# Performance work log

Measured on AMD Instinct MI355X. Metric: run time of the kernel, lower is better.

The kernel has to match this reference:

```python
import jax, jax.numpy as jnp
import numpy as np

HIDDEN = 768
NHEADS = 12
HEAD = HIDDEN // NHEADS


def setup_inputs() -> dict:
    key = jax.random.key(0)
    ks = jax.random.split(key, 10)
    B, S = 32, 512
    s = 1.0 / np.sqrt(HIDDEN)
    return {
        "x": jax.random.normal(ks[0], (B, S, HIDDEN), jnp.float32),
        "additive_attention_mask": jnp.zeros((B, 1, 1, S), jnp.float32),
        "Wq": jax.random.normal(ks[1], (HIDDEN, HIDDEN), jnp.float32) * s,
        "bq": jnp.zeros((HIDDEN,), jnp.float32),
        "Wk": jax.random.normal(ks[2], (HIDDEN, HIDDEN), jnp.float32) * s,
        "bk": jnp.zeros((HIDDEN,), jnp.float32),
        "Wv": jax.random.normal(ks[3], (HIDDEN, HIDDEN), jnp.float32) * s,
        "bv": jnp.zeros((HIDDEN,), jnp.float32),
        "Wo": jax.random.normal(ks[4], (HIDDEN, HIDDEN), jnp.float32) * s,
        "bo": jnp.zeros((HIDDEN,), jnp.float32),
    }


def reference(x, additive_attention_mask, Wq, bq, Wk, bk, Wv, bv, Wo, bo):
    B, S, _ = x.shape
    # projections (dropout is identity in eval mode)
    q = (x @ Wq + bq).reshape(B, S, NHEADS, HEAD)
    k = (x @ Wk + bk).reshape(B, S, NHEADS, HEAD)
    v = (x @ Wv + bv).reshape(B, S, NHEADS, HEAD)
    scores = jnp.einsum('bqhd,bkhd->bhqk', q, k) / jnp.sqrt(jnp.float32(HEAD))
    scores = scores + additive_attention_mask  # broadcast [B,1,1,S]
    probs = jax.nn.softmax(scores, axis=-1)
    attn = jnp.einsum('bhqk,bkhd->bqhd', probs, v).reshape(B, S, HIDDEN)
    return attn @ Wo + bo
```

## Files before the change

### kernel.cpp

```cpp
#include <hip/hip_runtime.h>
#include <stdint.h>

typedef unsigned short u16;
typedef __attribute__((ext_vector_type(4))) float floatx4;
typedef __attribute__((ext_vector_type(8))) __bf16 bf16x8;

__device__ __forceinline__ u16 f2bf(float f) {
  uint32_t u = __float_as_uint(f);
  u += 0x7FFFu + ((u >> 16) & 1u);
  return (u16)(u >> 16);
}

__global__ __launch_bounds__(256) void cast_x_kernel(const float* __restrict__ x,
                                                     u16* __restrict__ out) {
  int i = blockIdx.x * 256 + threadIdx.x;
  const float4* p = (const float4*)x;
  float4 a = p[(size_t)i * 2];
  float4 b = p[(size_t)i * 2 + 1];
  uint32_t w0 = (uint32_t)f2bf(a.x) | ((uint32_t)f2bf(a.y) << 16);
  uint32_t w1 = (uint32_t)f2bf(a.z) | ((uint32_t)f2bf(a.w) << 16);
  uint32_t w2 = (uint32_t)f2bf(b.x) | ((uint32_t)f2bf(b.y) << 16);
  uint32_t w3 = (uint32_t)f2bf(b.z) | ((uint32_t)f2bf(b.w) << 16);
  *(uint4*)(out + (size_t)i * 8) = make_uint4(w0, w1, w2, w3);
}

__global__ __launch_bounds__(256) void prep_wqkv_kernel(
    const float* __restrict__ Wq, const float* __restrict__ Wk, const float* __restrict__ Wv,
    const float* __restrict__ bq, const float* __restrict__ bk, const float* __restrict__ bv,
    u16* __restrict__ Wt, float* __restrict__ bias) {
  int id = blockIdx.x * 256 + threadIdx.x;
  int n = id / 768, k = id - n * 768;
  const float* W; const float* bs; int nn;
  if (n < 768)       { W = Wq; bs = bq; nn = n; }
  else if (n < 1536) { W = Wk; bs = bk; nn = n - 768; }
  else               { W = Wv; bs = bv; nn = n - 1536; }
  Wt[id] = f2bf(W[(size_t)k * 768 + nn]);
  if (k == 0) bias[n] = bs[nn];
}

__global__ __launch_bounds__(256) void prep_wo_kernel(const float* __restrict__ Wo,
                                                      u16* __restrict__ Wt) {
  int id = blockIdx.x * 256 + threadIdx.x;
  int n = id / 768, k = id - n * 768;
  Wt[id] = f2bf(Wo[(size_t)k * 768 + n]);
}

__device__ __forceinline__ void gload16(const void* g, void* l) {
  __builtin_amdgcn_global_load_lds((const __attribute__((address_space(1))) void*)g,
                                   (__attribute__((address_space(3))) void*)l,
                                   16, 0, 0);
}

template <int OUTF32>
__global__ __launch_bounds__(256) void gemm_bt_kernel(
    const u16* __restrict__ A, const u16* __restrict__ Bt,
    const float* __restrict__ bias, void* __restrict__ Cv, int ldc) {
  __shared__ __align__(16) u16 Alds[128 * 32];
  __shared__ __align__(16) u16 Blds[128 * 32];
  const int m0 = blockIdx.x * 128, n0 = blockIdx.y * 128;
  const int tid = threadIdx.x;
  const int lane = tid & 63, wid = tid >> 6;
  const int wr = wid >> 1, wc = wid & 1;
  const int l15 = lane & 15, l4 = lane >> 4;

  floatx4 zz = {0.f, 0.f, 0.f, 0.f};
  floatx4 acc[4][4];
#pragma unroll
  for (int i = 0; i < 4; ++i)
#pragma unroll
    for (int j = 0; j < 4; ++j) acc[i][j] = zz;

  for (int kt = 0; kt < 768; kt += 32) {
#pragma unroll
    for (int c = 0; c < 2; ++c) {
      int idx = (wid * 2 + c) * 64 + lane;
      int row = idx >> 2, kc = idx & 3;
      gload16(A + (size_t)(m0 + row) * 768 + kt + kc * 8,
              (char*)Alds + (wid * 2 + c) * 1024);
      gload16(Bt + (size_t)(n0 + row) * 768 + kt + kc * 8,
              (char*)Blds + (wid * 2 + c) * 1024);
    }
    __syncthreads();
    bf16x8 af[4], bfr[4];
#pragma unroll
    for (int i = 0; i < 4; ++i) {
      af[i]  = *(const bf16x8*)&Alds[(wr * 64 + i * 16 + l15) * 32 + l4 * 8];
      bfr[i] = *(const bf16x8*)&Blds[(wc * 64 + i * 16 + l15) * 32 + l4 * 8];
    }
#pragma unroll
    for (int i = 0; i < 4; ++i)
#pragma unroll
      for (int j = 0; j < 4; ++j)
        acc[i][j] = __builtin_amdgcn_mfma_f32_16x16x32_bf16(af[i], bfr[j], acc[i][j], 0, 0, 0);
    __syncthreads();
  }

#pragma unroll
  for (int i = 0; i < 4; ++i) {
    int row = m0 + wr * 64 + i * 16 + l4 * 4;
#pragma unroll
    for (int j = 0; j < 4; ++j) {
      int col = n0 + wc * 64 + j * 16 + l15;
      float bv = bias[col];
#pragma unroll
      for (int r = 0; r < 4; ++r) {
        float v = acc[i][j][r] + bv;
        if (OUTF32) ((float*)Cv)[(size_t)(row + r) * ldc + col] = v;
        else        ((u16*)Cv)[(size_t)(row + r) * ldc + col] = f2bf(v);
      }
    }
  }
}

__global__ __launch_bounds__(512, 4) void attn_kernel(const u16* __restrict__ qkv,
                                                      const float* __restrict__ mask,
                                                      u16* __restrict__ ctx) {
  __shared__ __align__(16) char lds[34816];
  char* sK = lds;
  char* sV = lds + 16384;
  float* sM = (float*)(lds + 32768);

  const int bid = blockIdx.x;
  const int wg = (bid & 7) * 192 + (bid >> 3);
  const int qt = wg & 3;
  const int h = (wg >> 2) % 12;
  const int b = wg / 48;

  const int tid = threadIdx.x;
  const int lane = tid & 63, w = tid >> 6;
  const int l15 = lane & 15, l4 = lane >> 4;
  const int hi = lane >> 3, doct = lane & 7;

  const u16* base = qkv + (size_t)b * 512 * 2304 + h * 64;
  const u16* Qg = base;
  const u16* Kg = base + 768;
  const u16* Vg = base + 1536;

  const int csw = doct ^ hi;
  const int vp_ = w * 8 + hi;

  auto stageK = [&](int t) {
    const u16* src = Kg + (size_t)(t * 128 + w * 16) * 2304;
#pragma unroll
    for (int i = 0; i < 2; ++i)
      gload16(src + (size_t)(i * 8 + hi) * 2304 + csw * 8,
              sK + (w * 2 + i) * 1024);
  };
  uint4 vra, vrb;
  auto loadV = [&](int t) {
    const u16* vp = Vg + (size_t)(t * 128 + vp_ * 2) * 2304 + doct * 8;
    vra = *(const uint4*)vp;
    vrb = *(const uint4*)(vp + 2304);
  };
  auto writeV = [&]() {
    const u16* pa = (const u16*)&vra;
    const u16* pb = (const u16*)&vrb;
#pragma unroll
    for (int j = 0; j < 8; ++j) {
      int d = doct * 8 + j;
      uint32_t val = (uint32_t)pa[j] | ((uint32_t)pb[j] << 16);
      *(uint32_t*)(sV + d * 256 +
                   ((4 * vp_) ^ ((d & 7) << 4) ^ (((d >> 3) & 3) << 5))) = val;
    }
  };

  float mval = mask[(size_t)b * 512 + tid];
  stageK(0);
  loadV(0);
  const u16* qp = Qg + (size_t)(qt * 128 + w * 16 + l15) * 2304 + l4 * 8;
  bf16x8 qf0 = *(const bf16x8*)qp;
  bf16x8 qf1 = *(const bf16x8*)(qp + 32);
  sM[tid] = mval;
  writeV();
  asm volatile("s_waitcnt vmcnt(0) lgkmcnt(0)" ::: "memory");
  __builtin_amdgcn_sched_barrier(0);
  __builtin_amdgcn_s_barrier();

  floatx4 zz = {0.f, 0.f, 0.f, 0.f};
  floatx4 oacc[4];
#pragma unroll
  for (int da = 0; da < 4; ++da) oacc[da] = zz;
  float m_ = -1e30f, l_ = 0.f;

  const int kswz = (l15 & 7) << 4;
  const int src0 = l15 + 32 * (l4 & 1);
  const int src1 = src0 + 16;
  const bool csel = (l4 & 2) != 0;

  for (int t = 0; t < 4; ++t) {
    if (t < 3) loadV(t + 1);

    floatx4 sacc[8];
#pragma unroll
    for (int ct = 0; ct < 8; ++ct) sacc[ct] = zz;
#pragma unroll
    for (int ct = 0; ct < 8; ++ct) {
      const char* kr = sK + (ct * 16 + l15) * 128;
      bf16x8 k0 = *(const bf16x8*)(kr + ((16 * l4) ^ kswz));
      bf16x8 k1 = *(const bf16x8*)(kr + ((64 + 16 * l4) ^ kswz));
      sacc[ct] = __builtin_amdgcn_mfma_f32_16x16x32_bf16(k0, qf0, sacc[ct], 0, 0, 0);
      sacc[ct] = __builtin_amdgcn_mfma_f32_16x16x32_bf16(k1, qf1, sacc[ct], 0, 0, 0);
    }

    float pm = -1e30f;
#pragma unroll
    for (int ct = 0; ct < 8; ++ct) {
      floatx4 mv = *(const floatx4*)(sM + t * 128 + ct * 16 + l4 * 4);
#pragma unroll
      for (int j = 0; j < 4; ++j) {
        float v = sacc[ct][j] * 0.125f + mv[j];
        sacc[ct][j] = v;
        pm = fmaxf(pm, v);
      }
    }
    pm = fmaxf(pm, __shfl_xor(pm, 16, 64));
    pm = fmaxf(pm, __shfl_xor(pm, 32, 64));
    float nm = fmaxf(m_, pm);
    float sc = __expf(m_ - nm);
    m_ = nm;
    float ts = 0.f;
#pragma unroll
    for (int ct = 0; ct < 8; ++ct)
#pragma unroll
      for (int j = 0; j < 4; ++j) {
        float e = __expf(sacc[ct][j] - nm);
        sacc[ct][j] = e;
        ts += e;
      }
    ts += __shfl_xor(ts, 16, 64);
    ts += __shfl_xor(ts, 32, 64);
    l_ = l_ * sc + ts;
#pragma unroll
    for (int da = 0; da < 4; ++da)
#pragma unroll
      for (int j = 0; j < 4; ++j) oacc[da][j] *= sc;

    uint32_t pk[8][2];
#pragma unroll
    for (int ct = 0; ct < 8; ++ct) {
#pragma unroll
      for (int p = 0; p < 2; ++p) {
        uint32_t ua = __float_as_uint(sacc[ct][2 * p]) + 0x8000u;
        uint32_t ub = __float_as_uint(sacc[ct][2 * p + 1]) + 0x8000u;
        pk[ct][p] = (ua >> 16) | (ub & 0xFFFF0000u);
      }
    }

#pragma unroll
    for (int ks = 0; ks < 4; ++ks) {
      uint32_t A0 = __shfl((int)pk[2 * ks][0], src0, 64);
      uint32_t B0 = __shfl((int)pk[2 * ks + 1][0], src0, 64);
      uint32_t A1 = __shfl((int)pk[2 * ks][1], src0, 64);
      uint32_t B1 = __shfl((int)pk[2 * ks + 1][1], src0, 64);
      uint32_t A2 = __shfl((int)pk[2 * ks][0], src1, 64);
      uint32_t B2 = __shfl((int)pk[2 * ks + 1][0], src1, 64);
      uint32_t A3 = __shfl((int)pk[2 * ks][1], src1, 64);
      uint32_t B3 = __shfl((int)pk[2 * ks + 1][1], src1, 64);
      union { uint32_t u[4]; bf16x8 v; } pf;
      pf.u[0] = csel ? B0 : A0;
      pf.u[1] = csel ? B1 : A1;
      pf.u[2] = csel ? B2 : A2;
      pf.u[3] = csel ? B3 : A3;
#pragma unroll
      for (int da = 0; da < 4; ++da) {
        int dd = da * 16 + l15;
        bf16x8 vf = *(const bf16x8*)(sV + dd * 256 +
            ((64 * ks + 16 * l4) ^ ((dd & 7) << 4) ^ (((dd >> 3) & 3) << 5)));
        oacc[da] = __builtin_amdgcn_mfma_f32_16x16x32_bf16(vf, pf.v, oacc[da], 0, 0, 0);
      }
    }

    asm volatile("s_waitcnt lgkmcnt(0)" ::: "memory");
    __builtin_amdgcn_sched_barrier(0);
    __builtin_amdgcn_s_barrier();
    if (t < 3) {
      stageK(t + 1);
      writeV();
      asm volatile("s_waitcnt vmcnt(0) lgkmcnt(0)" ::: "memory");
      __builtin_amdgcn_sched_barrier(0);
      __builtin_amdgcn_s_barrier();
    }
  }

  float rl = 1.0f / l_;
  u16* op = ctx + ((size_t)b * 512 + qt * 128 + w * 16 + l15) * 768 + h * 64;
#pragma unroll
  for (int da = 0; da < 4; ++da) {
    ushort4 o;
    o.x = f2bf(oacc[da][0] * rl);
    o.y = f2bf(oacc[da][1] * rl);
    o.z = f2bf(oacc[da][2] * rl);
    o.w = f2bf(oacc[da][3] * rl);
    *(ushort4*)(op + da * 16 + l4 * 4) = o;
  }
}

extern "C" void kernel_launch(void* const* d_in, const int* in_sizes, int n_in,
                              void* d_out, int out_size, void* d_ws, size_t ws_size,
                              hipStream_t stream) {
  const float* x    = (const float*)d_in[0];
  const float* mask = (const float*)d_in[1];
  const float* Wq   = (const float*)d_in[2];
  const float* bq   = (const float*)d_in[3];
  const float* Wk   = (const float*)d_in[4];
  const float* bk   = (const float*)d_in[5];
  const float* Wv   = (const float*)d_in[6];
  const float* bv   = (const float*)d_in[7];
  const float* Wo   = (const float*)d_in[8];
  const float* bo   = (const float*)d_in[9];
  float* out = (float*)d_out;

  char* ws = (char*)d_ws;
  u16*   xb   = (u16*)ws;
  u16*   ctx  = (u16*)(ws + 25165824);
  u16*   qkv  = (u16*)(ws + 50331648);
  u16*   wtq  = (u16*)(ws + 125829120);
  u16*   wto  = (u16*)(ws + 129368064);
  float* bqkv = (float*)(ws + 130547712);

  cast_x_kernel<<<6144, 256, 0, stream>>>(x, xb);
  prep_wqkv_kernel<<<6912, 256, 0, stream>>>(Wq, Wk, Wv, bq, bk, bv, wtq, bqkv);
  prep_wo_kernel<<<2304, 256, 0, stream>>>(Wo, wto);
  gemm_bt_kernel<0><<<dim3(128, 18), 256, 0, stream>>>(xb, wtq, bqkv, (void*)qkv, 2304);
  attn_kernel<<<dim3(1536), dim3(512), 0, stream>>>(qkv, mask, ctx);
  gemm_bt_kernel<1><<<dim3(128, 6), 256, 0, stream>>>(ctx, wto, bo, (void*)out, 768);
}
```

Measured before the change: 190.6 us.

## Replace GEMM with 256x256-tile, 4-stage pipelined, swizzled-LDS kernel

Replaces the 128x128 single-buffered GEMM with a 256x256 tile kernel of 512 threads. It uses a 4-deep ring of LDS buffers filled by direct global-to-LDS loads, prefetches three k-tiles ahead, and waits with explicit vmcnt so loads overlap MFMA work. It also adds an XOR swizzle on LDS chunks to avoid bank conflicts, XCD-aware block remapping, and raised s_setprio around the MFMA bursts. The larger tiles give more data reuse per load, but they use 128KB of LDS per block and more accumulator registers, and they leave fewer blocks for the 768-wide output projection (192 blocks).

```diff
diff --git a/kernel.cpp b/kernel.cpp
--- a/kernel.cpp
+++ b/kernel.cpp
@@ -52,59 +52,99 @@
 }
 
 template <int OUTF32>
-__global__ __launch_bounds__(256) void gemm_bt_kernel(
+__global__ __launch_bounds__(512, 2) void gemm256_kernel(
     const u16* __restrict__ A, const u16* __restrict__ Bt,
-    const float* __restrict__ bias, void* __restrict__ Cv, int ldc) {
-  __shared__ __align__(16) u16 Alds[128 * 32];
-  __shared__ __align__(16) u16 Blds[128 * 32];
-  const int m0 = blockIdx.x * 128, n0 = blockIdx.y * 128;
+    const float* __restrict__ bias, void* __restrict__ Cv, int ldc, int nt_count) {
+  __shared__ __align__(16) char lds[131072];
+
+  const int bid = blockIdx.x;
+  const int cpx = gridDim.x >> 3;
+  const int swz = (bid & 7) * cpx + (bid >> 3);
+  const int nt = swz % nt_count, mt = swz / nt_count;
+  const int m0 = mt * 256, n0 = nt * 256;
+
   const int tid = threadIdx.x;
-  const int lane = tid & 63, wid = tid >> 6;
-  const int wr = wid >> 1, wc = wid & 1;
+  const int lane = tid & 63, w = tid >> 6;
+  const int wr = w >> 2, wc = w & 3;
   const int l15 = lane & 15, l4 = lane >> 4;
+  const int srow = lane >> 2;
+  const int csw8 = ((lane & 3) ^ (srow & 3)) * 8;
+  const int achk = (l4 ^ (l15 & 3)) << 4;
+
+  auto stage = [&](int tile, int op) {
+    const u16* srcb = (op ? Bt + (size_t)n0 * 768 : A + (size_t)m0 * 768) + tile * 32;
+    char* dstb = lds + (tile & 3) * 32768 + op * 16384;
+#pragma unroll
+    for (int i = 0; i < 2; ++i) {
+      int r = (w * 2 + i) * 16 + srow;
+      gload16(srcb + (size_t)r * 768 + csw8, dstb + (w * 2 + i) * 1024);
+    }
+  };
 
   floatx4 zz = {0.f, 0.f, 0.f, 0.f};
-  floatx4 acc[4][4];
-#pragma unroll
-  for (int i = 0; i < 4; ++i)
+  floatx4 acc[8][4];
+#pragma unroll
+  for (int i = 0; i < 8; ++i)
 #pragma unroll
     for (int j = 0; j < 4; ++j) acc[i][j] = zz;
 
-  for (int kt = 0; kt < 768; kt += 32) {
-#pragma unroll
-    for (int c = 0; c < 2; ++c) {
-      int idx = (wid * 2 + c) * 64 + lane;
-      int row = idx >> 2, kc = idx & 3;
-      gload16(A + (size_t)(m0 + row) * 768 + kt + kc * 8,
-              (char*)Alds + (wid * 2 + c) * 1024);
-      gload16(Bt + (size_t)(n0 + row) * 768 + kt + kc * 8,
-              (char*)Blds + (wid * 2 + c) * 1024);
-    }
-    __syncthreads();
-    bf16x8 af[4], bfr[4];
-#pragma unroll
-    for (int i = 0; i < 4; ++i) {
-      af[i]  = *(const bf16x8*)&Alds[(wr * 64 + i * 16 + l15) * 32 + l4 * 8];
-      bfr[i] = *(const bf16x8*)&Blds[(wc * 64 + i * 16 + l15) * 32 + l4 * 8];
-    }
-#pragma unroll
-    for (int i = 0; i < 4; ++i)
-#pragma unroll
-      for (int j = 0; j < 4; ++j)
-        acc[i][j] = __builtin_amdgcn_mfma_f32_16x16x32_bf16(af[i], bfr[j], acc[i][j], 0, 0, 0);
-    __syncthreads();
-  }
-
-#pragma unroll
-  for (int i = 0; i < 4; ++i) {
-    int row = m0 + wr * 64 + i * 16 + l4 * 4;
-#pragma unroll
-    for (int j = 0; j < 4; ++j) {
-      int col = n0 + wc * 64 + j * 16 + l15;
+  stage(0, 0); stage(0, 1);
+  stage(1, 0); stage(1, 1);
+  stage(2, 0); stage(2, 1);
+  asm volatile("s_waitcnt vmcnt(8)" ::: "memory");
+  __builtin_amdgcn_sched_barrier(0);
+  __builtin_amdgcn_s_barrier();
+
+  bf16x8 bf[4];
+
+#define GPHASE(T, S, DOSTAGE, VM)                                                     \
+  {                                                                                   \
+    const char* bufA = lds + ((T) & 3) * 32768;                                       \
+    const char* bufB = bufA + 16384;                                                  \
+    bf16x8 af[4];                                                                     \
+    _Pragma("unroll") for (int mf = 0; mf < 4; ++mf)                                  \
+      af[mf] = *(const bf16x8*)(bufA +                                                \
+          (wr * 128 + (S) * 64 + mf * 16 + l15) * 64 + achk);                         \
+    if ((S) == 0) {                                                                   \
+      _Pragma("unroll") for (int nf = 0; nf < 4; ++nf)                                \
+        bf[nf] = *(const bf16x8*)(bufB + (wc * 64 + nf * 16 + l15) * 64 + achk);      \
+    }                                                                                 \
+    if (DOSTAGE) stage((T) + 3, (S));                                                 \
+    __builtin_amdgcn_sched_barrier(0);                                                \
+    __builtin_amdgcn_s_barrier();                                                     \
+    __builtin_amdgcn_s_setprio(1);                                                    \
+    _Pragma("unroll") for (int mf = 0; mf < 4; ++mf)                                  \
+      _Pragma("unroll") for (int nf = 0; nf < 4; ++nf)                                \
+        acc[(S) * 4 + mf][nf] = __builtin_amdgcn_mfma_f32_16x16x32_bf16(              \
+            af[mf], bf[nf], acc[(S) * 4 + mf][nf], 0, 0, 0);                          \
+    __builtin_amdgcn_s_setprio(0);                                                    \
+    VM;                                                                               \
+    __builtin_amdgcn_sched_barrier(0);                                                \
+    __builtin_amdgcn_s_barrier();                                                     \
+  }
+
+  for (int t = 0; t < 21; ++t) {
+    GPHASE(t, 0, true, (void)0)
+    GPHASE(t, 1, true, asm volatile("s_waitcnt vmcnt(8)" ::: "memory"))
+  }
+  GPHASE(21, 0, false, (void)0)
+  GPHASE(21, 1, false, asm volatile("s_waitcnt vmcnt(4)" ::: "memory"))
+  GPHASE(22, 0, false, (void)0)
+  GPHASE(22, 1, false, asm volatile("s_waitcnt vmcnt(0)" ::: "memory"))
+  GPHASE(23, 0, false, (void)0)
+  GPHASE(23, 1, false, (void)0)
+#undef GPHASE
+
+#pragma unroll
+  for (int ai = 0; ai < 8; ++ai) {
+    int row = m0 + wr * 128 + ai * 16 + l4 * 4;
+#pragma unroll
+    for (int nf = 0; nf < 4; ++nf) {
+      int col = n0 + wc * 64 + nf * 16 + l15;
       float bv = bias[col];
 #pragma unroll
       for (int r = 0; r < 4; ++r) {
-        float v = acc[i][j][r] + bv;
+        float v = acc[ai][nf][r] + bv;
         if (OUTF32) ((float*)Cv)[(size_t)(row + r) * ldc + col] = v;
         else        ((u16*)Cv)[(size_t)(row + r) * ldc + col] = f2bf(v);
       }
@@ -321,7 +361,7 @@
   cast_x_kernel<<<6144, 256, 0, stream>>>(x, xb);
   prep_wqkv_kernel<<<6912, 256, 0, stream>>>(Wq, Wk, Wv, bq, bk, bv, wtq, bqkv);
   prep_wo_kernel<<<2304, 256, 0, stream>>>(Wo, wto);
-  gemm_bt_kernel<0><<<dim3(128, 18), 256, 0, stream>>>(xb, wtq, bqkv, (void*)qkv, 2304);
+  gemm256_kernel<0><<<576, 512, 0, stream>>>(xb, wtq, bqkv, (void*)qkv, 2304, 9);
   attn_kernel<<<dim3(1536), dim3(512), 0, stream>>>(qkv, mask, ctx);
-  gemm_bt_kernel<1><<<dim3(128, 6), 256, 0, stream>>>(ctx, wto, bo, (void*)out, 768);
-}
+  gemm256_kernel<1><<<192, 512, 0, stream>>>(ctx, wto, bo, (void*)out, 768, 3);
+}
```

New measurement: 197.8 us. 3.8% more time.

## Double GEMM K-tile with XOR-swizzled LDS and fuse weight transposes via shared memory

Applied to the files above, without the earlier changes.

The GEMM now loads a 64-wide K slice per iteration instead of 32, which halves the barrier count per tile. It stores the slice in LDS with an XOR swizzle to avoid bank conflicts on the 128-byte rows, and sets a 4-blocks-per-CU launch bound. The separate Wqkv and Wo prep kernels are merged into one tiled transpose kernel that stages data through shared memory, giving coalesced reads and writes in place of strided global reads. The larger LDS tiles double shared memory per block, which may limit occupancy.

```diff
diff --git a/kernel.cpp b/kernel.cpp
--- a/kernel.cpp
+++ b/kernel.cpp
@@ -24,25 +24,37 @@
   *(uint4*)(out + (size_t)i * 8) = make_uint4(w0, w1, w2, w3);
 }
 
-__global__ __launch_bounds__(256) void prep_wqkv_kernel(
-    const float* __restrict__ Wq, const float* __restrict__ Wk, const float* __restrict__ Wv,
+__global__ __launch_bounds__(256) void prep_w_kernel(
+    const float* __restrict__ Wq, const float* __restrict__ Wk,
+    const float* __restrict__ Wv, const float* __restrict__ Wo,
     const float* __restrict__ bq, const float* __restrict__ bk, const float* __restrict__ bv,
-    u16* __restrict__ Wt, float* __restrict__ bias) {
-  int id = blockIdx.x * 256 + threadIdx.x;
-  int n = id / 768, k = id - n * 768;
-  const float* W; const float* bs; int nn;
-  if (n < 768)       { W = Wq; bs = bq; nn = n; }
-  else if (n < 1536) { W = Wk; bs = bk; nn = n - 768; }
-  else               { W = Wv; bs = bv; nn = n - 1536; }
-  Wt[id] = f2bf(W[(size_t)k * 768 + nn]);
-  if (k == 0) bias[n] = bs[nn];
-}
-
-__global__ __launch_bounds__(256) void prep_wo_kernel(const float* __restrict__ Wo,
-                                                      u16* __restrict__ Wt) {
-  int id = blockIdx.x * 256 + threadIdx.x;
-  int n = id / 768, k = id - n * 768;
-  Wt[id] = f2bf(Wo[(size_t)k * 768 + n]);
+    u16* __restrict__ Wt, u16* __restrict__ Wto, float* __restrict__ bias) {
+  __shared__ u16 sT[64][72];
+  const int kt = blockIdx.x * 64, nt = blockIdx.y * 64, mat = blockIdx.z;
+  const float* W = mat == 0 ? Wq : mat == 1 ? Wk : mat == 2 ? Wv : Wo;
+  const int tid = threadIdx.x;
+  const int r = tid >> 2, c4 = tid & 3;
+#pragma unroll
+  for (int p = 0; p < 4; ++p) {
+    int c = c4 * 16 + p * 4;
+    float4 v = *(const float4*)&W[(size_t)(kt + r) * 768 + nt + c];
+    sT[c + 0][r] = f2bf(v.x);
+    sT[c + 1][r] = f2bf(v.y);
+    sT[c + 2][r] = f2bf(v.z);
+    sT[c + 3][r] = f2bf(v.w);
+  }
+  __syncthreads();
+  const int n = tid >> 2, kq = tid & 3;
+  uint4 o0 = *(const uint4*)&sT[n][kq * 16];
+  uint4 o1 = *(const uint4*)&sT[n][kq * 16 + 8];
+  u16* dst = (mat < 3 ? Wt + ((size_t)(mat * 768 + nt + n)) * 768
+                      : Wto + (size_t)(nt + n) * 768) + kt + kq * 16;
+  *(uint4*)dst = o0;
+  *(uint4*)(dst + 8) = o1;
+  if (mat < 3 && blockIdx.x == 0 && tid < 64) {
+    const float* bs = mat == 0 ? bq : mat == 1 ? bk : bv;
+    bias[mat * 768 + nt + tid] = bs[nt + tid];
+  }
 }
 
 __device__ __forceinline__ void gload16(const void* g, void* l) {
@@ -52,16 +64,18 @@
 }
 
 template <int OUTF32>
-__global__ __launch_bounds__(256) void gemm_bt_kernel(
+__global__ __launch_bounds__(256, 4) void gemm_bt_kernel(
     const u16* __restrict__ A, const u16* __restrict__ Bt,
     const float* __restrict__ bias, void* __restrict__ Cv, int ldc) {
-  __shared__ __align__(16) u16 Alds[128 * 32];
-  __shared__ __align__(16) u16 Blds[128 * 32];
+  __shared__ __align__(16) u16 Alds[128 * 64];
+  __shared__ __align__(16) u16 Blds[128 * 64];
   const int m0 = blockIdx.x * 128, n0 = blockIdx.y * 128;
   const int tid = threadIdx.x;
   const int lane = tid & 63, wid = tid >> 6;
   const int wr = wid >> 1, wc = wid & 1;
   const int l15 = lane & 15, l4 = lane >> 4;
+  const int srow = lane >> 3;
+  const int csw = (lane & 7) ^ srow;
 
   floatx4 zz = {0.f, 0.f, 0.f, 0.f};
   floatx4 acc[4][4];
@@ -70,28 +84,31 @@
 #pragma unroll
     for (int j = 0; j < 4; ++j) acc[i][j] = zz;
 
-  for (int kt = 0; kt < 768; kt += 32) {
-#pragma unroll
-    for (int c = 0; c < 2; ++c) {
-      int idx = (wid * 2 + c) * 64 + lane;
-      int row = idx >> 2, kc = idx & 3;
-      gload16(A + (size_t)(m0 + row) * 768 + kt + kc * 8,
-              (char*)Alds + (wid * 2 + c) * 1024);
-      gload16(Bt + (size_t)(n0 + row) * 768 + kt + kc * 8,
-              (char*)Blds + (wid * 2 + c) * 1024);
+  for (int kt = 0; kt < 768; kt += 64) {
+#pragma unroll
+    for (int i = 0; i < 4; ++i) {
+      int u = wid * 4 + i;
+      int row = u * 8 + srow;
+      gload16(A + (size_t)(m0 + row) * 768 + kt + csw * 8, (char*)Alds + u * 1024);
+      gload16(Bt + (size_t)(n0 + row) * 768 + kt + csw * 8, (char*)Blds + u * 1024);
     }
     __syncthreads();
-    bf16x8 af[4], bfr[4];
-#pragma unroll
-    for (int i = 0; i < 4; ++i) {
-      af[i]  = *(const bf16x8*)&Alds[(wr * 64 + i * 16 + l15) * 32 + l4 * 8];
-      bfr[i] = *(const bf16x8*)&Blds[(wc * 64 + i * 16 + l15) * 32 + l4 * 8];
-    }
-#pragma unroll
-    for (int i = 0; i < 4; ++i)
-#pragma unroll
-      for (int j = 0; j < 4; ++j)
-        acc[i][j] = __builtin_amdgcn_mfma_f32_16x16x32_bf16(af[i], bfr[j], acc[i][j], 0, 0, 0);
+#pragma unroll
+    for (int kk = 0; kk < 2; ++kk) {
+      bf16x8 af[4], bfr[4];
+#pragma unroll
+      for (int i = 0; i < 4; ++i) {
+        int ra = wr * 64 + i * 16 + l15;
+        int rb = wc * 64 + i * 16 + l15;
+        af[i]  = *(const bf16x8*)((char*)Alds + ra * 128 + (((kk * 4 + l4) ^ (l15 & 7)) << 4));
+        bfr[i] = *(const bf16x8*)((char*)Blds + rb * 128 + (((kk * 4 + l4) ^ (l15 & 7)) << 4));
+      }
+#pragma unroll
+      for (int i = 0; i < 4; ++i)
+#pragma unroll
+        for (int j = 0; j < 4; ++j)
+          acc[i][j] = __builtin_amdgcn_mfma_f32_16x16x32_bf16(af[i], bfr[j], acc[i][j], 0, 0, 0);
+    }
     __syncthreads();
   }
 
@@ -319,8 +336,8 @@
   float* bqkv = (float*)(ws + 130547712);
 
   cast_x_kernel<<<6144, 256, 0, stream>>>(x, xb);
-  prep_wqkv_kernel<<<6912, 256, 0, stream>>>(Wq, Wk, Wv, bq, bk, bv, wtq, bqkv);
-  prep_wo_kernel<<<2304, 256, 0, stream>>>(Wo, wto);
+  prep_w_kernel<<<dim3(12, 12, 4), 256, 0, stream>>>(Wq, Wk, Wv, Wo, bq, bk, bv,
+                                                     wtq, wto, bqkv);
   gemm_bt_kernel<0><<<dim3(128, 18), 256, 0, stream>>>(xb, wtq, bqkv, (void*)qkv, 2304);
   attn_kernel<<<dim3(1536), dim3(512), 0, stream>>>(qkv, mask, ctx);
   gemm_bt_kernel<1><<<dim3(128, 6), 256, 0, stream>>>(ctx, wto, bo, (void*)out, 768);
```

After: 162.0 us. -15.0%, faster.
